# Optimization experiments

Hardware: AMD Instinct MI355X
Metric: run time of the kernel (lower is better)

The kernel has to match this reference:

```python
import jax, jax.numpy as jnp
import numpy as np

W_RNN = 768
DEC_H = 256
TAGS = 2
TAG_EM = 32


def setup_inputs() -> dict:
    key = jax.random.key(0)
    ks = jax.random.split(key, 8)
    B, T = 64, 512
    in_size = W_RNN + TAG_EM  # 800
    aff_in = W_RNN + DEC_H    # 1024
    sents_vec = jax.random.normal(ks[0], (B, T, W_RNN), dtype=jnp.float32)
    mask_cls = jnp.ones((B, T), dtype=jnp.float32)
    # xavier-uniform-ish init for weights, zeros for biases (matches param_init)
    def xavier(k, shape):
        fan_in, fan_out = shape[1], shape[0]
        lim = float(np.sqrt(6.0 / (fan_in + fan_out)))
        return jax.random.uniform(k, shape, jnp.float32, -lim, lim)
    Wih = xavier(ks[1], (4 * DEC_H, in_size))
    Whh = xavier(ks[2], (4 * DEC_H, DEC_H))
    bih = jnp.zeros((4 * DEC_H,), jnp.float32)
    bhh = jnp.zeros((4 * DEC_H,), jnp.float32)
    Waff = xavier(ks[3], (TAGS, aff_in))
    baff = jnp.zeros((TAGS,), jnp.float32)
    tag_em = xavier(ks[4], (TAGS, TAG_EM))
    return {"sents_vec": sents_vec, "mask_cls": mask_cls, "Wih": Wih,
            "Whh": Whh, "bih": bih, "bhh": bhh, "Waff": Waff,
            "baff": baff, "tag_em": tag_em}


def reference(sents_vec, mask_cls, Wih, Whh, bih, bhh, Waff, baff, tag_em):
    # Dropout is treated in eval mode (identity), as is standard for a
    # deterministic correctness baseline.
    B, T, D = sents_vec.shape
    H = DEC_H
    h0 = jnp.zeros((B, H), sents_vec.dtype)
    go = jnp.zeros((B, TAG_EM), sents_vec.dtype)

    Hs = jnp.swapaxes(sents_vec, 0, 1)        # [T, B, D]
    Ms = jnp.swapaxes(mask_cls, 0, 1)[..., None]  # [T, B, 1]

    def step(carry, xs):
        h, c, yem = carry
        Hi, mi = xs
        x = jnp.concatenate([yem, Hi], axis=1)            # [B, 800]
        gates = x @ Wih.T + h @ Whh.T + (bih + bhh)       # [B, 4H]
        i_g, f_g, g_g, o_g = jnp.split(gates, 4, axis=1)  # torch LSTMCell order
        c_new = jax.nn.sigmoid(f_g) * c + jax.nn.sigmoid(i_g) * jnp.tanh(g_g)
        h_new = jax.nn.sigmoid(o_g) * jnp.tanh(c_new)
        score = jnp.concatenate([h_new, Hi], axis=1) @ Waff.T + baff  # [B, TAGS]
        pred = jnp.argmax(score, axis=-1)                 # [B]
        yem_new = tag_em[pred]                            # [B, TAG_EM]
        h_out = h_new * mi + h * (1.0 - mi)
        c_out = c_new * mi + c * (1.0 - mi)
        return (h_out, c_out, yem_new), score

    _, scores = jax.lax.scan(step, (h0, h0, go), (Hs, Ms))  # [T, B, TAGS]
    scores = jnp.swapaxes(scores, 0, 1)                      # [B, T, TAGS]
    return jax.nn.log_softmax(scores, axis=2)
```

## Files before the change

### kernel.cpp

```cpp
#include <hip/hip_runtime.h>
#include <cstdint>
#include <cstddef>

#define TT 512
#define BB 64
#define HH 256
#define NG 1024
#define DI 768
#define KY 32

#define LDP 56

typedef __attribute__((ext_vector_type(8))) short bfrag_t;
typedef __attribute__((ext_vector_type(4))) float f4_t;

__device__ __forceinline__ float sigf(float x) {
    return __fdividef(1.f, 1.f + __expf(-x));
}
__device__ __forceinline__ float tanhfast(float x) {
    return fmaf(2.f, sigf(2.f * x), -1.f);
}
__device__ __forceinline__ unsigned short bf_hi(float x) {
    return (unsigned short)(__float_as_uint(x) >> 16);
}
__device__ __forceinline__ float bf_hi_f(float x) {
    return __uint_as_float(__float_as_uint(x) & 0xffff0000u);
}

__global__ __launch_bounds__(256) void kgemm2(
    const float* __restrict__ sents, const float* __restrict__ Wih,
    const float* __restrict__ bih, const float* __restrict__ bhh,
    float* __restrict__ gpre, int t0)
{
    __shared__ unsigned short Ah[128 * LDP], Al[128 * LDP];
    __shared__ unsigned short Bh[128 * LDP], Bl[128 * LDP];

    const int tid = threadIdx.x;
    const int nb = blockIdx.x;
    const int mb = blockIdx.y;
    const int wv = tid >> 6, lane = tid & 63;
    const int wm = (wv >> 1) * 64, wn = (wv & 1) * 64;
    const int fl = lane & 15, quad = lane >> 4;

    f4_t acc[4][4];
#pragma unroll
    for (int mi = 0; mi < 4; ++mi)
#pragma unroll
        for (int ni = 0; ni < 4; ++ni) acc[mi][ni] = (f4_t)0.f;

    const int sr = tid >> 1, sk = (tid & 1) * 16;
    const int gr = mb * 128 + sr;
    const float* aptr = sents + ((size_t)(gr & 63) * TT + t0 + (gr >> 6)) * DI + sk;
    const float* bptr = Wih + (size_t)(nb * 128 + sr) * 800 + KY + sk;

    for (int k0 = 0; k0 < DI; k0 += 32) {
        float4 av[4], bv[4];
#pragma unroll
        for (int i = 0; i < 4; ++i) {
            av[i] = *(const float4*)(aptr + k0 + i * 4);
            bv[i] = *(const float4*)(bptr + k0 + i * 4);
        }
        __syncthreads();
#pragma unroll
        for (int i = 0; i < 4; ++i) {
            ushort4 h4, l4;
            h4.x = bf_hi(av[i].x); l4.x = bf_hi(av[i].x - bf_hi_f(av[i].x));
            h4.y = bf_hi(av[i].y); l4.y = bf_hi(av[i].y - bf_hi_f(av[i].y));
            h4.z = bf_hi(av[i].z); l4.z = bf_hi(av[i].z - bf_hi_f(av[i].z));
            h4.w = bf_hi(av[i].w); l4.w = bf_hi(av[i].w - bf_hi_f(av[i].w));
            *(ushort4*)&Ah[sr * LDP + sk + i * 4] = h4;
            *(ushort4*)&Al[sr * LDP + sk + i * 4] = l4;
            h4.x = bf_hi(bv[i].x); l4.x = bf_hi(bv[i].x - bf_hi_f(bv[i].x));
            h4.y = bf_hi(bv[i].y); l4.y = bf_hi(bv[i].y - bf_hi_f(bv[i].y));
            h4.z = bf_hi(bv[i].z); l4.z = bf_hi(bv[i].z - bf_hi_f(bv[i].z));
            h4.w = bf_hi(bv[i].w); l4.w = bf_hi(bv[i].w - bf_hi_f(bv[i].w));
            *(ushort4*)&Bh[sr * LDP + sk + i * 4] = h4;
            *(ushort4*)&Bl[sr * LDP + sk + i * 4] = l4;
        }
        __syncthreads();

        bfrag_t ah[4], al2[4], bh[4], bl2[4];
#pragma unroll
        for (int mi = 0; mi < 4; ++mi) {
            int row = wm + mi * 16 + fl;
            ah[mi]  = *(const bfrag_t*)&Ah[row * LDP + quad * 8];
            al2[mi] = *(const bfrag_t*)&Al[row * LDP + quad * 8];
        }
#pragma unroll
        for (int ni = 0; ni < 4; ++ni) {
            int col = wn + ni * 16 + fl;
            bh[ni]  = *(const bfrag_t*)&Bh[col * LDP + quad * 8];
            bl2[ni] = *(const bfrag_t*)&Bl[col * LDP + quad * 8];
        }
#pragma unroll
        for (int mi = 0; mi < 4; ++mi)
#pragma unroll
            for (int ni = 0; ni < 4; ++ni) {
                acc[mi][ni] = __builtin_amdgcn_mfma_f32_16x16x32_bf16(
                    ah[mi], bh[ni], acc[mi][ni], 0, 0, 0);
                acc[mi][ni] = __builtin_amdgcn_mfma_f32_16x16x32_bf16(
                    ah[mi], bl2[ni], acc[mi][ni], 0, 0, 0);
                acc[mi][ni] = __builtin_amdgcn_mfma_f32_16x16x32_bf16(
                    al2[mi], bh[ni], acc[mi][ni], 0, 0, 0);
            }
    }

#pragma unroll
    for (int ni = 0; ni < 4; ++ni) {
        int gcol = nb * 128 + wn + ni * 16 + fl;
        float bias = bih[gcol] + bhh[gcol];
#pragma unroll
        for (int mi = 0; mi < 4; ++mi) {
            int grow = mb * 128 + wm + mi * 16 + quad * 4;
#pragma unroll
            for (int r = 0; r < 4; ++r)
                gpre[(size_t)(grow + r) * NG + gcol] = acc[mi][ni][r] + bias;
        }
    }
}

__global__ __launch_bounds__(256) void kshi(
    const float* __restrict__ sents, const float* __restrict__ Waff,
    const float* __restrict__ baff, float* __restrict__ shi, int t0)
{
    const int tid = threadIdx.x;
    const int lane = tid & 63;
    const int r = blockIdx.x * 4 + (tid >> 6);
    const int b = r & 63, tl = r >> 6;
    const float* hi = sents + ((size_t)b * TT + t0 + tl) * DI;
    float p0 = 0.f, p1 = 0.f;
#pragma unroll
    for (int kk = 0; kk < 12; ++kk) {
        int k = kk * 64 + lane;
        float x = hi[k];
        p0 = fmaf(x, Waff[HH + k], p0);
        p1 = fmaf(x, Waff[NG + HH + k], p1);
    }
#pragma unroll
    for (int off = 32; off >= 1; off >>= 1) {
        p0 += __shfl_xor(p0, off, 64);
        p1 += __shfl_xor(p1, off, 64);
    }
    if (lane == 0) {
        shi[(size_t)r * 2 + 0] = p0 + baff[0];
        shi[(size_t)r * 2 + 1] = p1 + baff[1];
    }
}

__global__ void kinit(unsigned long long* __restrict__ hbox) {
    hbox[(size_t)blockIdx.x * 512 + threadIdx.x] = 0ull;
}

__global__ __launch_bounds__(512, 1) void krec4(
    const float* __restrict__ gpre,
    const float* __restrict__ shi,
    const float* __restrict__ Whh,
    const float* __restrict__ mask,
    float* __restrict__ out,
    float* __restrict__ sh, float* __restrict__ sc, int* __restrict__ sp,
    unsigned long long* __restrict__ hbox,
    const float* __restrict__ Wih, const float* __restrict__ tag,
    const float* __restrict__ Waff,
    int t0, int Tc, int first)
{
    const int blk = blockIdx.x;
    const int g = blk >> 6, b = blk & 63;
    const int tid = threadIdx.x;
    const int w = tid >> 6, lane = tid & 63;
    const int jl = lane & 7, kq = lane >> 3;
    const int jh = w * 8 + jl;
    const int jglob = g * 64 + jh;

    __shared__ float hbl[2][8 * 36];
    __shared__ float hraw[2][8 * 36];
    __shared__ float P[2][4][64];
    __shared__ float tg[2][KY];

    float4 wreg[4][8];
#pragma unroll
    for (int gt = 0; gt < 4; ++gt) {
        const float4* src = (const float4*)(Whh + (size_t)(gt * HH + jglob) * HH + kq * 32);
#pragma unroll
        for (int kk = 0; kk < 8; ++kk) wreg[gt][kk] = src[kk];
    }

    const float4 wf0 = *(const float4*)(Waff + 4 * lane);
    const float4 wf1 = *(const float4*)(Waff + NG + 4 * lane);

    if (tid < 2 * KY) tg[tid >> 5][tid & 31] = tag[tid];
    __syncthreads();
    {
        int r = tid >> 8, rem = tid & 255, gt = rem >> 6, j2 = rem & 63;
        int row = gt * HH + g * 64 + j2;
        const float4* wr = (const float4*)(Wih + (size_t)row * 800);
        float s = 0.f;
#pragma unroll
        for (int kk = 0; kk < 8; ++kk) {
            float4 v = wr[kk];
            s = fmaf(v.x, tg[r][kk * 4 + 0], s);
            s = fmaf(v.y, tg[r][kk * 4 + 1], s);
            s = fmaf(v.z, tg[r][kk * 4 + 2], s);
            s = fmaf(v.w, tg[r][kk * 4 + 3], s);
        }
        P[r][gt][j2] = s;
    }

    const int gpg = (g + 1 + (tid >> 6)) & 3;
    const int gj2 = tid & 63;

    float creg, hblreg = 0.f, gblreg = 0.f;
    int pred;
    if (first) {
        creg = 0.f; pred = -1;
        if (tid < 256) hbl[0][(tid >> 5) * 36 + (tid & 31)] = 0.f;
    } else {
        creg = sc[(size_t)b * HH + jglob];
        pred = sp[b];
        if (kq == 0)   hblreg = sh[(size_t)b * HH + jglob];
        if (tid < 192) gblreg = sh[(size_t)b * HH + gpg * 64 + gj2];
        if (tid < 256) hbl[0][(tid >> 5) * 36 + (tid & 31)] = sh[(size_t)b * HH + tid];
    }
    __syncthreads();

    float cgp0, cgp1, cgp2, cgp3, cmi, cs0, cs1;
    {
        const float* gp = gpre + (size_t)b * NG;
        cgp0 = gp[0 * HH + jglob]; cgp1 = gp[1 * HH + jglob];
        cgp2 = gp[2 * HH + jglob]; cgp3 = gp[3 * HH + jglob];
        cmi = mask[(size_t)b * TT + t0];
        const float* s2 = shi + (size_t)b * 2;
        cs0 = s2[0]; cs1 = s2[1];
    }
    float sc0p = 0.f, sc1p = 0.f;

    for (int tl = 0; tl < Tc; ++tl) {
        const int t = t0 + tl;
        const int rp = tl & 1;
        const int wp2 = rp ^ 1;
        const int hp = t & 1;

        if (tl > 0) {
            float4 hv = *(const float4*)(&hraw[rp][(lane >> 3) * 36 + (lane & 7) * 4]);
            float s0 = hv.x * wf0.x;
            s0 = fmaf(hv.y, wf0.y, s0); s0 = fmaf(hv.z, wf0.z, s0); s0 = fmaf(hv.w, wf0.w, s0);
            float s1 = hv.x * wf1.x;
            s1 = fmaf(hv.y, wf1.y, s1); s1 = fmaf(hv.z, wf1.z, s1); s1 = fmaf(hv.w, wf1.w, s1);
#pragma unroll
            for (int off = 1; off <= 32; off <<= 1) {
                s0 += __shfl_xor(s0, off, 64);
                s1 += __shfl_xor(s1, off, 64);
            }
            float ts0 = s0 + sc0p, ts1 = s1 + sc1p;
            pred = (ts1 > ts0) ? 1 : 0;
            if (g == 0 && tid == 0) {
                float m = fmaxf(ts0, ts1);
                float lse = m + log1pf(expf(-fabsf(ts0 - ts1)));
                float* op = out + ((size_t)b * TT + (t - 1)) * 2;
                op[0] = ts0 - lse; op[1] = ts1 - lse;
            }
        }

        float a0 = 0.f, a1 = 0.f, a2 = 0.f, a3 = 0.f;
        const float4* h4 = (const float4*)(&hbl[rp][kq * 36]);
#pragma unroll
        for (int kk = 0; kk < 8; ++kk) {
            float4 hv = h4[kk];
            a0 = fmaf(wreg[0][kk].x, hv.x, a0); a0 = fmaf(wreg[0][kk].y, hv.y, a0);
            a0 = fmaf(wreg[0][kk].z, hv.z, a0); a0 = fmaf(wreg[0][kk].w, hv.w, a0);
            a1 = fmaf(wreg[1][kk].x, hv.x, a1); a1 = fmaf(wreg[1][kk].y, hv.y, a1);
            a1 = fmaf(wreg[1][kk].z, hv.z, a1); a1 = fmaf(wreg[1][kk].w, hv.w, a1);
            a2 = fmaf(wreg[2][kk].x, hv.x, a2); a2 = fmaf(wreg[2][kk].y, hv.y, a2);
            a2 = fmaf(wreg[2][kk].z, hv.z, a2); a2 = fmaf(wreg[2][kk].w, hv.w, a2);
            a3 = fmaf(wreg[3][kk].x, hv.x, a3); a3 = fmaf(wreg[3][kk].y, hv.y, a3);
            a3 = fmaf(wreg[3][kk].z, hv.z, a3); a3 = fmaf(wreg[3][kk].w, hv.w, a3);
        }
        a0 += __shfl_xor(a0, 8, 64); a0 += __shfl_xor(a0, 16, 64); a0 += __shfl_xor(a0, 32, 64);
        a1 += __shfl_xor(a1, 8, 64); a1 += __shfl_xor(a1, 16, 64); a1 += __shfl_xor(a1, 32, 64);
        a2 += __shfl_xor(a2, 8, 64); a2 += __shfl_xor(a2, 16, 64); a2 += __shfl_xor(a2, 32, 64);
        a3 += __shfl_xor(a3, 8, 64); a3 += __shfl_xor(a3, 16, 64); a3 += __shfl_xor(a3, 32, 64);

        float pv0 = 0.f, pv1 = 0.f, pv2 = 0.f, pv3 = 0.f;
        if (pred >= 0) {
            pv0 = P[pred][0][jh]; pv1 = P[pred][1][jh];
            pv2 = P[pred][2][jh]; pv3 = P[pred][3][jh];
        }

        float gi = a0 + cgp0 + pv0;
        float gf = a1 + cgp1 + pv1;
        float gg = a2 + cgp2 + pv2;
        float go = a3 + cgp3 + pv3;
        float ig = sigf(gi), fg = sigf(gf);
        float g2 = tanhfast(gg), og = sigf(go);
        float cn = fmaf(fg, creg, ig * g2);
        float hn = og * tanhfast(cn);
        const float mi = cmi;
        creg = fmaf(cn - creg, mi, creg);

        if (kq == 0) {
            hblreg = fmaf(hn - hblreg, mi, hblreg);
            const int ji = (jglob >> 5) * 36 + (jglob & 31);
            hraw[wp2][ji] = hn;
            hbl[wp2][ji]  = hblreg;
            unsigned long long wd =
                ((unsigned long long)__float_as_uint(hn) << 32) | (unsigned)(t + 1);
            __hip_atomic_store(&hbox[((size_t)(hp * BB + b) * 4 + g) * 64 + jh], wd,
                               __ATOMIC_RELAXED, __HIP_MEMORY_SCOPE_AGENT);
        }

        sc0p = cs0; sc1p = cs1;
        if (tl + 1 < Tc) {
            const float* gp2 = gpre + ((size_t)(tl + 1) * BB + b) * NG;
            cgp0 = gp2[0 * HH + jglob]; cgp1 = gp2[1 * HH + jglob];
            cgp2 = gp2[2 * HH + jglob]; cgp3 = gp2[3 * HH + jglob];
            cmi = mask[(size_t)b * TT + t + 1];
            const float* s2n = shi + ((size_t)(tl + 1) * BB + b) * 2;
            cs0 = s2n[0]; cs1 = s2n[1];
        }

        if (tid < 192) {
            const unsigned long long* wpt =
                &hbox[((size_t)(hp * BB + b) * 4 + gpg) * 64 + gj2];
            unsigned long long wv;
            do {
                wv = __hip_atomic_load(wpt, __ATOMIC_RELAXED, __HIP_MEMORY_SCOPE_AGENT);
            } while ((unsigned)wv != (unsigned)(t + 1));
            float raw = __uint_as_float((unsigned)(wv >> 32));
            gblreg = fmaf(raw - gblreg, mi, gblreg);
            const int ji = gpg * 64 + gj2;
            const int jj = (ji >> 5) * 36 + (ji & 31);
            hraw[wp2][jj] = raw;
            hbl[wp2][jj]  = gblreg;
        }
        __syncthreads();
    }

    {
        const int rp = Tc & 1;
        float4 hv = *(const float4*)(&hraw[rp][(lane >> 3) * 36 + (lane & 7) * 4]);
        float s0 = hv.x * wf0.x;
        s0 = fmaf(hv.y, wf0.y, s0); s0 = fmaf(hv.z, wf0.z, s0); s0 = fmaf(hv.w, wf0.w, s0);
        float s1 = hv.x * wf1.x;
        s1 = fmaf(hv.y, wf1.y, s1); s1 = fmaf(hv.z, wf1.z, s1); s1 = fmaf(hv.w, wf1.w, s1);
#pragma unroll
        for (int off = 1; off <= 32; off <<= 1) {
            s0 += __shfl_xor(s0, off, 64);
            s1 += __shfl_xor(s1, off, 64);
        }
        float ts0 = s0 + sc0p, ts1 = s1 + sc1p;
        pred = (ts1 > ts0) ? 1 : 0;
        if (g == 0 && tid == 0) {
            float m = fmaxf(ts0, ts1);
            float lse = m + log1pf(expf(-fabsf(ts0 - ts1)));
            float* op = out + ((size_t)b * TT + (t0 + Tc - 1)) * 2;
            op[0] = ts0 - lse; op[1] = ts1 - lse;
        }
    }
    if (kq == 0) {
        sh[(size_t)b * HH + jglob] = hblreg;
        sc[(size_t)b * HH + jglob] = creg;
    }
    if (g == 0 && tid == 0) sp[b] = pred;
}

extern "C" void kernel_launch(void* const* d_in, const int* in_sizes, int n_in,
                              void* d_out, int out_size, void* d_ws, size_t ws_size,
                              hipStream_t stream) {
    (void)in_sizes; (void)n_in; (void)out_size;
    const float* sents = (const float*)d_in[0];
    const float* mask  = (const float*)d_in[1];
    const float* Wih   = (const float*)d_in[2];
    const float* Whh   = (const float*)d_in[3];
    const float* bih   = (const float*)d_in[4];
    const float* bhh   = (const float*)d_in[5];
    const float* Waff  = (const float*)d_in[6];
    const float* baff  = (const float*)d_in[7];
    const float* tag   = (const float*)d_in[8];
    float* out = (float*)d_out;

    const size_t fixed = (size_t)BB * HH * 4 * 2
                       + BB * 4
                       + (size_t)2 * BB * 4 * 64 * 8
                       + 4096;
    int Tc = 8;
    const int cands[7] = {512, 256, 128, 64, 32, 16, 8};
    for (int i = 0; i < 7; ++i) {
        size_t need = (size_t)cands[i] * BB * NG * 4
                    + (size_t)cands[i] * BB * 2 * 4
                    + fixed;
        if (need <= ws_size) { Tc = cands[i]; break; }
    }

    char* wsp = (char*)d_ws;
    float* gpre = (float*)wsp; wsp += (size_t)Tc * BB * NG * 4;
    float* shiw = (float*)wsp; wsp += (size_t)Tc * BB * 2 * 4;
    float* shst = (float*)wsp; wsp += (size_t)BB * HH * 4;
    float* scst = (float*)wsp; wsp += (size_t)BB * HH * 4;
    int*   spst = (int*)wsp;   wsp += BB * 4;
    unsigned long long* hbox = (unsigned long long*)wsp;

    kinit<<<dim3(64), 512, 0, stream>>>(hbox);

    const int nch = TT / Tc;
    for (int c = 0; c < nch; ++c) {
        const int t0 = c * Tc;
        kgemm2<<<dim3(8, Tc * 64 / 128), 256, 0, stream>>>(sents, Wih, bih, bhh, gpre, t0);
        kshi<<<dim3(Tc * 16), 256, 0, stream>>>(sents, Waff, baff, shiw, t0);
        krec4<<<dim3(256), 512, 0, stream>>>(gpre, shiw, Whh, mask, out,
                                             shst, scst, spst, hbox,
                                             Wih, tag, Waff, t0, Tc, (c == 0) ? 1 : 0);
    }
}
```

Before: 1.480 ms.

## Process two batch rows per recurrent block, halving the grid

The recurrent kernel now handles two batch rows per block (b and b+32) with 128 blocks instead of 256, reusing the register-resident Whh slice for both rows. Blocks now publish both the raw and the masked hidden value in the mailbox, so consumers no longer recompute the masked value, and the mailbox and its init grow to match. This doubles per-block serial work per step but halves the number of cross-block spinning participants and the global spin traffic. The shi score load was also moved so it indexes by the current step.

New measurement: 2.134 ms. +44.2%, slower.

```diff
diff --git a/kernel.cpp b/kernel.cpp
--- a/kernel.cpp
+++ b/kernel.cpp
@@ -151,7 +151,7 @@
     hbox[(size_t)blockIdx.x * 512 + threadIdx.x] = 0ull;
 }
 
-__global__ __launch_bounds__(512, 1) void krec4(
+__global__ __launch_bounds__(512, 1) void krec5(
     const float* __restrict__ gpre,
     const float* __restrict__ shi,
     const float* __restrict__ Whh,
@@ -164,15 +164,17 @@
     int t0, int Tc, int first)
 {
     const int blk = blockIdx.x;
-    const int g = blk >> 6, b = blk & 63;
+    const int g = blk >> 5;
+    const int b0 = blk & 31;
+    const int b1 = b0 + 32;
     const int tid = threadIdx.x;
     const int w = tid >> 6, lane = tid & 63;
     const int jl = lane & 7, kq = lane >> 3;
     const int jh = w * 8 + jl;
     const int jglob = g * 64 + jh;
 
-    __shared__ float hbl[2][8 * 36];
-    __shared__ float hraw[2][8 * 36];
+    __shared__ float hbl0[2][8 * 36], hraw0[2][8 * 36];
+    __shared__ float hbl1[2][8 * 36], hraw1[2][8 * 36];
     __shared__ float P[2][4][64];
     __shared__ float tg[2][KY];
 
@@ -205,33 +207,43 @@
         P[r][gt][j2] = s;
     }
 
-    const int gpg = (g + 1 + (tid >> 6)) & 3;
-    const int gj2 = tid & 63;
-
-    float creg, hblreg = 0.f, gblreg = 0.f;
-    int pred;
+    const int gt0 = tid;
+    const int gt1 = tid - 192;
+    const int pg0 = (g + 1 + (gt0 >> 6)) & 3, pj0 = gt0 & 63;
+    const int pg1 = (g + 1 + (gt1 >> 6)) & 3, pj1 = gt1 & 63;
+
+    float creg0, creg1, hblreg0 = 0.f, hblreg1 = 0.f;
+    int pred0, pred1;
     if (first) {
-        creg = 0.f; pred = -1;
-        if (tid < 256) hbl[0][(tid >> 5) * 36 + (tid & 31)] = 0.f;
+        creg0 = 0.f; creg1 = 0.f; pred0 = -1; pred1 = -1;
+        if (tid < 256) hbl0[0][(tid >> 5) * 36 + (tid & 31)] = 0.f;
+        else { int q = tid - 256; hbl1[0][(q >> 5) * 36 + (q & 31)] = 0.f; }
     } else {
-        creg = sc[(size_t)b * HH + jglob];
-        pred = sp[b];
-        if (kq == 0)   hblreg = sh[(size_t)b * HH + jglob];
-        if (tid < 192) gblreg = sh[(size_t)b * HH + gpg * 64 + gj2];
-        if (tid < 256) hbl[0][(tid >> 5) * 36 + (tid & 31)] = sh[(size_t)b * HH + tid];
+        creg0 = sc[(size_t)b0 * HH + jglob];
+        creg1 = sc[(size_t)b1 * HH + jglob];
+        pred0 = sp[b0]; pred1 = sp[b1];
+        if (kq == 0) {
+            hblreg0 = sh[(size_t)b0 * HH + jglob];
+            hblreg1 = sh[(size_t)b1 * HH + jglob];
+        }
+        if (tid < 256) hbl0[0][(tid >> 5) * 36 + (tid & 31)] = sh[(size_t)b0 * HH + tid];
+        else { int q = tid - 256; hbl1[0][(q >> 5) * 36 + (q & 31)] = sh[(size_t)b1 * HH + q]; }
     }
     __syncthreads();
 
-    float cgp0, cgp1, cgp2, cgp3, cmi, cs0, cs1;
+    float cgp00, cgp01, cgp02, cgp03, cmi0;
+    float cgp10, cgp11, cgp12, cgp13, cmi1;
     {
-        const float* gp = gpre + (size_t)b * NG;
-        cgp0 = gp[0 * HH + jglob]; cgp1 = gp[1 * HH + jglob];
-        cgp2 = gp[2 * HH + jglob]; cgp3 = gp[3 * HH + jglob];
-        cmi = mask[(size_t)b * TT + t0];
-        const float* s2 = shi + (size_t)b * 2;
-        cs0 = s2[0]; cs1 = s2[1];
-    }
-    float sc0p = 0.f, sc1p = 0.f;
+        const float* gp0 = gpre + (size_t)b0 * NG;
+        cgp00 = gp0[0 * HH + jglob]; cgp01 = gp0[1 * HH + jglob];
+        cgp02 = gp0[2 * HH + jglob]; cgp03 = gp0[3 * HH + jglob];
+        const float* gp1 = gpre + (size_t)b1 * NG;
+        cgp10 = gp1[0 * HH + jglob]; cgp11 = gp1[1 * HH + jglob];
+        cgp12 = gp1[2 * HH + jglob]; cgp13 = gp1[3 * HH + jglob];
+        cmi0 = mask[(size_t)b0 * TT + t0];
+        cmi1 = mask[(size_t)b1 * TT + t0];
+    }
+    float sc00 = 0.f, sc01 = 0.f, sc10 = 0.f, sc11 = 0.f;
 
     for (int tl = 0; tl < Tc; ++tl) {
         const int t = t0 + tl;
@@ -240,126 +252,222 @@
         const int hp = t & 1;
 
         if (tl > 0) {
-            float4 hv = *(const float4*)(&hraw[rp][(lane >> 3) * 36 + (lane & 7) * 4]);
-            float s0 = hv.x * wf0.x;
-            s0 = fmaf(hv.y, wf0.y, s0); s0 = fmaf(hv.z, wf0.z, s0); s0 = fmaf(hv.w, wf0.w, s0);
-            float s1 = hv.x * wf1.x;
-            s1 = fmaf(hv.y, wf1.y, s1); s1 = fmaf(hv.z, wf1.z, s1); s1 = fmaf(hv.w, wf1.w, s1);
+            const int so = (lane >> 3) * 36 + (lane & 7) * 4;
+            float4 hv0 = *(const float4*)(&hraw0[rp][so]);
+            float4 hv1 = *(const float4*)(&hraw1[rp][so]);
+            float s0a = hv0.x * wf0.x, s1a = hv0.x * wf1.x;
+            s0a = fmaf(hv0.y, wf0.y, s0a); s0a = fmaf(hv0.z, wf0.z, s0a); s0a = fmaf(hv0.w, wf0.w, s0a);
+            s1a = fmaf(hv0.y, wf1.y, s1a); s1a = fmaf(hv0.z, wf1.z, s1a); s1a = fmaf(hv0.w, wf1.w, s1a);
+            float s0b = hv1.x * wf0.x, s1b = hv1.x * wf1.x;
+            s0b = fmaf(hv1.y, wf0.y, s0b); s0b = fmaf(hv1.z, wf0.z, s0b); s0b = fmaf(hv1.w, wf0.w, s0b);
+            s1b = fmaf(hv1.y, wf1.y, s1b); s1b = fmaf(hv1.z, wf1.z, s1b); s1b = fmaf(hv1.w, wf1.w, s1b);
 #pragma unroll
             for (int off = 1; off <= 32; off <<= 1) {
-                s0 += __shfl_xor(s0, off, 64);
-                s1 += __shfl_xor(s1, off, 64);
-            }
-            float ts0 = s0 + sc0p, ts1 = s1 + sc1p;
-            pred = (ts1 > ts0) ? 1 : 0;
+                s0a += __shfl_xor(s0a, off, 64); s1a += __shfl_xor(s1a, off, 64);
+                s0b += __shfl_xor(s0b, off, 64); s1b += __shfl_xor(s1b, off, 64);
+            }
+            float t00 = s0a + sc00, t01 = s1a + sc01;
+            float t10 = s0b + sc10, t11 = s1b + sc11;
+            pred0 = (t01 > t00) ? 1 : 0;
+            pred1 = (t11 > t10) ? 1 : 0;
             if (g == 0 && tid == 0) {
-                float m = fmaxf(ts0, ts1);
-                float lse = m + log1pf(expf(-fabsf(ts0 - ts1)));
-                float* op = out + ((size_t)b * TT + (t - 1)) * 2;
-                op[0] = ts0 - lse; op[1] = ts1 - lse;
-            }
-        }
-
-        float a0 = 0.f, a1 = 0.f, a2 = 0.f, a3 = 0.f;
-        const float4* h4 = (const float4*)(&hbl[rp][kq * 36]);
-#pragma unroll
-        for (int kk = 0; kk < 8; ++kk) {
-            float4 hv = h4[kk];
-            a0 = fmaf(wreg[0][kk].x, hv.x, a0); a0 = fmaf(wreg[0][kk].y, hv.y, a0);
-            a0 = fmaf(wreg[0][kk].z, hv.z, a0); a0 = fmaf(wreg[0][kk].w, hv.w, a0);
-            a1 = fmaf(wreg[1][kk].x, hv.x, a1); a1 = fmaf(wreg[1][kk].y, hv.y, a1);
-            a1 = fmaf(wreg[1][kk].z, hv.z, a1); a1 = fmaf(wreg[1][kk].w, hv.w, a1);
-            a2 = fmaf(wreg[2][kk].x, hv.x, a2); a2 = fmaf(wreg[2][kk].y, hv.y, a2);
-            a2 = fmaf(wreg[2][kk].z, hv.z, a2); a2 = fmaf(wreg[2][kk].w, hv.w, a2);
-            a3 = fmaf(wreg[3][kk].x, hv.x, a3); a3 = fmaf(wreg[3][kk].y, hv.y, a3);
-            a3 = fmaf(wreg[3][kk].z, hv.z, a3); a3 = fmaf(wreg[3][kk].w, hv.w, a3);
-        }
-        a0 += __shfl_xor(a0, 8, 64); a0 += __shfl_xor(a0, 16, 64); a0 += __shfl_xor(a0, 32, 64);
-        a1 += __shfl_xor(a1, 8, 64); a1 += __shfl_xor(a1, 16, 64); a1 += __shfl_xor(a1, 32, 64);
-        a2 += __shfl_xor(a2, 8, 64); a2 += __shfl_xor(a2, 16, 64); a2 += __shfl_xor(a2, 32, 64);
-        a3 += __shfl_xor(a3, 8, 64); a3 += __shfl_xor(a3, 16, 64); a3 += __shfl_xor(a3, 32, 64);
-
-        float pv0 = 0.f, pv1 = 0.f, pv2 = 0.f, pv3 = 0.f;
-        if (pred >= 0) {
-            pv0 = P[pred][0][jh]; pv1 = P[pred][1][jh];
-            pv2 = P[pred][2][jh]; pv3 = P[pred][3][jh];
-        }
-
-        float gi = a0 + cgp0 + pv0;
-        float gf = a1 + cgp1 + pv1;
-        float gg = a2 + cgp2 + pv2;
-        float go = a3 + cgp3 + pv3;
-        float ig = sigf(gi), fg = sigf(gf);
-        float g2 = tanhfast(gg), og = sigf(go);
-        float cn = fmaf(fg, creg, ig * g2);
-        float hn = og * tanhfast(cn);
-        const float mi = cmi;
-        creg = fmaf(cn - creg, mi, creg);
-
-        if (kq == 0) {
-            hblreg = fmaf(hn - hblreg, mi, hblreg);
-            const int ji = (jglob >> 5) * 36 + (jglob & 31);
-            hraw[wp2][ji] = hn;
-            hbl[wp2][ji]  = hblreg;
-            unsigned long long wd =
-                ((unsigned long long)__float_as_uint(hn) << 32) | (unsigned)(t + 1);
-            __hip_atomic_store(&hbox[((size_t)(hp * BB + b) * 4 + g) * 64 + jh], wd,
-                               __ATOMIC_RELAXED, __HIP_MEMORY_SCOPE_AGENT);
-        }
-
-        sc0p = cs0; sc1p = cs1;
+                float m0 = fmaxf(t00, t01);
+                float l0 = m0 + log1pf(expf(-fabsf(t00 - t01)));
+                float* op0 = out + ((size_t)b0 * TT + (t - 1)) * 2;
+                op0[0] = t00 - l0; op0[1] = t01 - l0;
+                float m1 = fmaxf(t10, t11);
+                float l1 = m1 + log1pf(expf(-fabsf(t10 - t11)));
+                float* op1 = out + ((size_t)b1 * TT + (t - 1)) * 2;
+                op1[0] = t10 - l1; op1[1] = t11 - l1;
+            }
+        }
+
+        {
+            float a0 = 0.f, a1 = 0.f, a2 = 0.f, a3 = 0.f;
+            const float4* h4 = (const float4*)(&hbl0[rp][kq * 36]);
+#pragma unroll
+            for (int kk = 0; kk < 8; ++kk) {
+                float4 hv = h4[kk];
+                a0 = fmaf(wreg[0][kk].x, hv.x, a0); a0 = fmaf(wreg[0][kk].y, hv.y, a0);
+                a0 = fmaf(wreg[0][kk].z, hv.z, a0); a0 = fmaf(wreg[0][kk].w, hv.w, a0);
+                a1 = fmaf(wreg[1][kk].x, hv.x, a1); a1 = fmaf(wreg[1][kk].y, hv.y, a1);
+                a1 = fmaf(wreg[1][kk].z, hv.z, a1); a1 = fmaf(wreg[1][kk].w, hv.w, a1);
+                a2 = fmaf(wreg[2][kk].x, hv.x, a2); a2 = fmaf(wreg[2][kk].y, hv.y, a2);
+                a2 = fmaf(wreg[2][kk].z, hv.z, a2); a2 = fmaf(wreg[2][kk].w, hv.w, a2);
+                a3 = fmaf(wreg[3][kk].x, hv.x, a3); a3 = fmaf(wreg[3][kk].y, hv.y, a3);
+                a3 = fmaf(wreg[3][kk].z, hv.z, a3); a3 = fmaf(wreg[3][kk].w, hv.w, a3);
+            }
+            a0 += __shfl_xor(a0, 8, 64); a0 += __shfl_xor(a0, 16, 64); a0 += __shfl_xor(a0, 32, 64);
+            a1 += __shfl_xor(a1, 8, 64); a1 += __shfl_xor(a1, 16, 64); a1 += __shfl_xor(a1, 32, 64);
+            a2 += __shfl_xor(a2, 8, 64); a2 += __shfl_xor(a2, 16, 64); a2 += __shfl_xor(a2, 32, 64);
+            a3 += __shfl_xor(a3, 8, 64); a3 += __shfl_xor(a3, 16, 64); a3 += __shfl_xor(a3, 32, 64);
+
+            float pv0 = 0.f, pv1 = 0.f, pv2 = 0.f, pv3 = 0.f;
+            if (pred0 >= 0) {
+                pv0 = P[pred0][0][jh]; pv1 = P[pred0][1][jh];
+                pv2 = P[pred0][2][jh]; pv3 = P[pred0][3][jh];
+            }
+            float gi = a0 + cgp00 + pv0;
+            float gf = a1 + cgp01 + pv1;
+            float gg = a2 + cgp02 + pv2;
+            float go = a3 + cgp03 + pv3;
+            float ig = sigf(gi), fg = sigf(gf);
+            float g2 = tanhfast(gg), og = sigf(go);
+            float cn = fmaf(fg, creg0, ig * g2);
+            float hn = og * tanhfast(cn);
+            creg0 = fmaf(cn - creg0, cmi0, creg0);
+
+            if (kq == 0) {
+                hblreg0 = fmaf(hn - hblreg0, cmi0, hblreg0);
+                const int ji = (jglob >> 5) * 36 + (jglob & 31);
+                hraw0[wp2][ji] = hn;
+                hbl0[wp2][ji] = hblreg0;
+                unsigned long long* pb =
+                    &hbox[(((size_t)(hp * BB + b0) * 4 + g) * 64 + jh) * 2];
+                unsigned long long w0 =
+                    ((unsigned long long)__float_as_uint(hn) << 32) | (unsigned)(t + 1);
+                unsigned long long w1 =
+                    ((unsigned long long)__float_as_uint(hblreg0) << 32) | (unsigned)(t + 1);
+                __hip_atomic_store(pb + 0, w0, __ATOMIC_RELAXED, __HIP_MEMORY_SCOPE_AGENT);
+                __hip_atomic_store(pb + 1, w1, __ATOMIC_RELAXED, __HIP_MEMORY_SCOPE_AGENT);
+            }
+        }
+
+        {
+            float a0 = 0.f, a1 = 0.f, a2 = 0.f, a3 = 0.f;
+            const float4* h4 = (const float4*)(&hbl1[rp][kq * 36]);
+#pragma unroll
+            for (int kk = 0; kk < 8; ++kk) {
+                float4 hv = h4[kk];
+                a0 = fmaf(wreg[0][kk].x, hv.x, a0); a0 = fmaf(wreg[0][kk].y, hv.y, a0);
+                a0 = fmaf(wreg[0][kk].z, hv.z, a0); a0 = fmaf(wreg[0][kk].w, hv.w, a0);
+                a1 = fmaf(wreg[1][kk].x, hv.x, a1); a1 = fmaf(wreg[1][kk].y, hv.y, a1);
+                a1 = fmaf(wreg[1][kk].z, hv.z, a1); a1 = fmaf(wreg[1][kk].w, hv.w, a1);
+                a2 = fmaf(wreg[2][kk].x, hv.x, a2); a2 = fmaf(wreg[2][kk].y, hv.y, a2);
+                a2 = fmaf(wreg[2][kk].z, hv.z, a2); a2 = fmaf(wreg[2][kk].w, hv.w, a2);
+                a3 = fmaf(wreg[3][kk].x, hv.x, a3); a3 = fmaf(wreg[3][kk].y, hv.y, a3);
+                a3 = fmaf(wreg[3][kk].w, hv.w, a3); a3 = fmaf(wreg[3][kk].z, hv.z, a3);
+            }
+            a0 += __shfl_xor(a0, 8, 64); a0 += __shfl_xor(a0, 16, 64); a0 += __shfl_xor(a0, 32, 64);
+            a1 += __shfl_xor(a1, 8, 64); a1 += __shfl_xor(a1, 16, 64); a1 += __shfl_xor(a1, 32, 64);
+            a2 += __shfl_xor(a2, 8, 64); a2 += __shfl_xor(a2, 16, 64); a2 += __shfl_xor(a2, 32, 64);
+            a3 += __shfl_xor(a3, 8, 64); a3 += __shfl_xor(a3, 16, 64); a3 += __shfl_xor(a3, 32, 64);
+
+            float pv0 = 0.f, pv1 = 0.f, pv2 = 0.f, pv3 = 0.f;
+            if (pred1 >= 0) {
+                pv0 = P[pred1][0][jh]; pv1 = P[pred1][1][jh];
+                pv2 = P[pred1][2][jh]; pv3 = P[pred1][3][jh];
+            }
+            float gi = a0 + cgp10 + pv0;
+            float gf = a1 + cgp11 + pv1;
+            float gg = a2 + cgp12 + pv2;
+            float go = a3 + cgp13 + pv3;
+            float ig = sigf(gi), fg = sigf(gf);
+            float g2 = tanhfast(gg), og = sigf(go);
+            float cn = fmaf(fg, creg1, ig * g2);
+            float hn = og * tanhfast(cn);
+            creg1 = fmaf(cn - creg1, cmi1, creg1);
+
+            if (kq == 0) {
+                hblreg1 = fmaf(hn - hblreg1, cmi1, hblreg1);
+                const int ji = (jglob >> 5) * 36 + (jglob & 31);
+                hraw1[wp2][ji] = hn;
+                hbl1[wp2][ji] = hblreg1;
+                unsigned long long* pb =
+                    &hbox[(((size_t)(hp * BB + b1) * 4 + g) * 64 + jh) * 2];
+                unsigned long long w0 =
+                    ((unsigned long long)__float_as_uint(hn) << 32) | (unsigned)(t + 1);
+                unsigned long long w1 =
+                    ((unsigned long long)__float_as_uint(hblreg1) << 32) | (unsigned)(t + 1);
+                __hip_atomic_store(pb + 0, w0, __ATOMIC_RELAXED, __HIP_MEMORY_SCOPE_AGENT);
+                __hip_atomic_store(pb + 1, w1, __ATOMIC_RELAXED, __HIP_MEMORY_SCOPE_AGENT);
+            }
+        }
+
+        {
+            const float* s20 = shi + ((size_t)tl * BB + b0) * 2;
+            const float* s21 = shi + ((size_t)tl * BB + b1) * 2;
+            sc00 = s20[0]; sc01 = s20[1];
+            sc10 = s21[0]; sc11 = s21[1];
+        }
         if (tl + 1 < Tc) {
-            const float* gp2 = gpre + ((size_t)(tl + 1) * BB + b) * NG;
-            cgp0 = gp2[0 * HH + jglob]; cgp1 = gp2[1 * HH + jglob];
-            cgp2 = gp2[2 * HH + jglob]; cgp3 = gp2[3 * HH + jglob];
-            cmi = mask[(size_t)b * TT + t + 1];
-            const float* s2n = shi + ((size_t)(tl + 1) * BB + b) * 2;
-            cs0 = s2n[0]; cs1 = s2n[1];
-        }
-
+            const float* gp0 = gpre + ((size_t)(tl + 1) * BB + b0) * NG;
+            cgp00 = gp0[0 * HH + jglob]; cgp01 = gp0[1 * HH + jglob];
+            cgp02 = gp0[2 * HH + jglob]; cgp03 = gp0[3 * HH + jglob];
+            const float* gp1 = gpre + ((size_t)(tl + 1) * BB + b1) * NG;
+            cgp10 = gp1[0 * HH + jglob]; cgp11 = gp1[1 * HH + jglob];
+            cgp12 = gp1[2 * HH + jglob]; cgp13 = gp1[3 * HH + jglob];
+            cmi0 = mask[(size_t)b0 * TT + t + 1];
+            cmi1 = mask[(size_t)b1 * TT + t + 1];
+        }
+
+        const unsigned T = (unsigned)(t + 1);
         if (tid < 192) {
-            const unsigned long long* wpt =
-                &hbox[((size_t)(hp * BB + b) * 4 + gpg) * 64 + gj2];
-            unsigned long long wv;
+            const unsigned long long* wq =
+                &hbox[(((size_t)(hp * BB + b0) * 4 + pg0) * 64 + pj0) * 2];
+            unsigned long long va, vb;
             do {
-                wv = __hip_atomic_load(wpt, __ATOMIC_RELAXED, __HIP_MEMORY_SCOPE_AGENT);
-            } while ((unsigned)wv != (unsigned)(t + 1));
-            float raw = __uint_as_float((unsigned)(wv >> 32));
-            gblreg = fmaf(raw - gblreg, mi, gblreg);
-            const int ji = gpg * 64 + gj2;
+                va = __hip_atomic_load(wq + 0, __ATOMIC_RELAXED, __HIP_MEMORY_SCOPE_AGENT);
+                vb = __hip_atomic_load(wq + 1, __ATOMIC_RELAXED, __HIP_MEMORY_SCOPE_AGENT);
+            } while ((unsigned)va != T || (unsigned)vb != T);
+            const int ji = pg0 * 64 + pj0;
             const int jj = (ji >> 5) * 36 + (ji & 31);
-            hraw[wp2][jj] = raw;
-            hbl[wp2][jj]  = gblreg;
+            hraw0[wp2][jj] = __uint_as_float((unsigned)(va >> 32));
+            hbl0[wp2][jj]  = __uint_as_float((unsigned)(vb >> 32));
+        } else if (tid < 384) {
+            const unsigned long long* wq =
+                &hbox[(((size_t)(hp * BB + b1) * 4 + pg1) * 64 + pj1) * 2];
+            unsigned long long va, vb;
+            do {
+                va = __hip_atomic_load(wq + 0, __ATOMIC_RELAXED, __HIP_MEMORY_SCOPE_AGENT);
+                vb = __hip_atomic_load(wq + 1, __ATOMIC_RELAXED, __HIP_MEMORY_SCOPE_AGENT);
+            } while ((unsigned)va != T || (unsigned)vb != T);
+            const int ji = pg1 * 64 + pj1;
+            const int jj = (ji >> 5) * 36 + (ji & 31);
+            hraw1[wp2][jj] = __uint_as_float((unsigned)(va >> 32));
+            hbl1[wp2][jj]  = __uint_as_float((unsigned)(vb >> 32));
         }
         __syncthreads();
     }
 
     {
         const int rp = Tc & 1;
-        float4 hv = *(const float4*)(&hraw[rp][(lane >> 3) * 36 + (lane & 7) * 4]);
-        float s0 = hv.x * wf0.x;
-        s0 = fmaf(hv.y, wf0.y, s0); s0 = fmaf(hv.z, wf0.z, s0); s0 = fmaf(hv.w, wf0.w, s0);
-        float s1 = hv.x * wf1.x;
-        s1 = fmaf(hv.y, wf1.y, s1); s1 = fmaf(hv.z, wf1.z, s1); s1 = fmaf(hv.w, wf1.w, s1);
+        const int so = (lane >> 3) * 36 + (lane & 7) * 4;
+        float4 hv0 = *(const float4*)(&hraw0[rp][so]);
+        float4 hv1 = *(const float4*)(&hraw1[rp][so]);
+        float s0a = hv0.x * wf0.x, s1a = hv0.x * wf1.x;
+        s0a = fmaf(hv0.y, wf0.y, s0a); s0a = fmaf(hv0.z, wf0.z, s0a); s0a = fmaf(hv0.w, wf0.w, s0a);
+        s1a = fmaf(hv0.y, wf1.y, s1a); s1a = fmaf(hv0.z, wf1.z, s1a); s1a = fmaf(hv0.w, wf1.w, s1a);
+        float s0b = hv1.x * wf0.x, s1b = hv1.x * wf1.x;
+        s0b = fmaf(hv1.y, wf0.y, s0b); s0b = fmaf(hv1.z, wf0.z, s0b); s0b = fmaf(hv1.w, wf0.w, s0b);
+        s1b = fmaf(hv1.y, wf1.y, s1b); s1b = fmaf(hv1.z, wf1.z, s1b); s1b = fmaf(hv1.w, wf1.w, s1b);
 #pragma unroll
         for (int off = 1; off <= 32; off <<= 1) {
-            s0 += __shfl_xor(s0, off, 64);
-            s1 += __shfl_xor(s1, off, 64);
-        }
-        float ts0 = s0 + sc0p, ts1 = s1 + sc1p;
-        pred = (ts1 > ts0) ? 1 : 0;
+            s0a += __shfl_xor(s0a, off, 64); s1a += __shfl_xor(s1a, off, 64);
+            s0b += __shfl_xor(s0b, off, 64); s1b += __shfl_xor(s1b, off, 64);
+        }
+        float t00 = s0a + sc00, t01 = s1a + sc01;
+        float t10 = s0b + sc10, t11 = s1b + sc11;
+        pred0 = (t01 > t00) ? 1 : 0;
+        pred1 = (t11 > t10) ? 1 : 0;
         if (g == 0 && tid == 0) {
-            float m = fmaxf(ts0, ts1);
-            float lse = m + log1pf(expf(-fabsf(ts0 - ts1)));
-            float* op = out + ((size_t)b * TT + (t0 + Tc - 1)) * 2;
-            op[0] = ts0 - lse; op[1] = ts1 - lse;
+            float m0 = fmaxf(t00, t01);
+            float l0 = m0 + log1pf(expf(-fabsf(t00 - t01)));
+            float* op0 = out + ((size_t)b0 * TT + (t0 + Tc - 1)) * 2;
+            op0[0] = t00 - l0; op0[1] = t01 - l0;
+            float m1 = fmaxf(t10, t11);
+            float l1 = m1 + log1pf(expf(-fabsf(t10 - t11)));
+            float* op1 = out + ((size_t)b1 * TT + (t0 + Tc - 1)) * 2;
+            op1[0] = t10 - l1; op1[1] = t11 - l1;
         }
     }
     if (kq == 0) {
-        sh[(size_t)b * HH + jglob] = hblreg;
-        sc[(size_t)b * HH + jglob] = creg;
-    }
-    if (g == 0 && tid == 0) sp[b] = pred;
+        sh[(size_t)b0 * HH + jglob] = hblreg0;
+        sc[(size_t)b0 * HH + jglob] = creg0;
+        sh[(size_t)b1 * HH + jglob] = hblreg1;
+        sc[(size_t)b1 * HH + jglob] = creg1;
+    }
+    if (g == 0 && tid == 0) { sp[b0] = pred0; sp[b1] = pred1; }
 }
 
 extern "C" void kernel_launch(void* const* d_in, const int* in_sizes, int n_in,
@@ -379,7 +487,7 @@
 
     const size_t fixed = (size_t)BB * HH * 4 * 2
                        + BB * 4
-                       + (size_t)2 * BB * 4 * 64 * 8
+                       + (size_t)2 * BB * 4 * 64 * 2 * 8
                        + 4096;
     int Tc = 8;
     const int cands[7] = {512, 256, 128, 64, 32, 16, 8};
@@ -398,14 +506,14 @@
     int*   spst = (int*)wsp;   wsp += BB * 4;
     unsigned long long* hbox = (unsigned long long*)wsp;
 
-    kinit<<<dim3(64), 512, 0, stream>>>(hbox);
+    kinit<<<dim3(128), 512, 0, stream>>>(hbox);
 
     const int nch = TT / Tc;
     for (int c = 0; c < nch; ++c) {
         const int t0 = c * Tc;
         kgemm2<<<dim3(8, Tc * 64 / 128), 256, 0, stream>>>(sents, Wih, bih, bhh, gpre, t0);
         kshi<<<dim3(Tc * 16), 256, 0, stream>>>(sents, Waff, baff, shiw, t0);
-        krec4<<<dim3(256), 512, 0, stream>>>(gpre, shiw, Whh, mask, out,
+        krec5<<<dim3(128), 512, 0, stream>>>(gpre, shiw, Whh, mask, out,
                                              shst, scst, spst, hbox,
                                              Wih, tag, Waff, t0, Tc, (c == 0) ? 1 : 0);
     }
```
